# Optimization experiments

Measured on AMD Instinct MI355X. Metric: run time of the kernel, lower is better.

Reference implementation:

```python
import jax, jax.numpy as jnp
import numpy as np

B = 16      # number of point clouds
N = 4096    # points per cloud (max segment size, static)
D = 3       # xyz


def setup_inputs() -> dict:
    key = jax.random.key(0)
    k1, k2 = jax.random.split(key)
    pred = jax.random.normal(k1, (B * N, D), dtype=jnp.float32)
    target = jax.random.normal(k2, (B * N, D), dtype=jnp.float32)
    # sorted batch assignment with equal-size segments (so N_max is static)
    batch = jnp.repeat(jnp.arange(B, dtype=jnp.int64), N)
    return {"pred": pred, "target": target, "batch": batch}


def _to_dense_batch(x, batch):
    # Faithful to torch_geometric.utils.to_dense_batch: scatter each point into
    # its (cloud, within-cloud-position) slot; padding slots stay zero.
    T = x.shape[0]
    counts = jax.ops.segment_sum(jnp.ones((T,), jnp.int32), batch, num_segments=B)
    starts = jnp.concatenate([jnp.zeros((1,), jnp.int32), jnp.cumsum(counts)[:-1]])
    pos = jnp.arange(T, dtype=jnp.int32) - starts[batch]
    dense = jnp.zeros((B, N, x.shape[1]), x.dtype).at[batch, pos].set(x)
    return dense


def _chamfer(x, y):
    # pytorch3d.loss.chamfer_distance defaults: squared L2, point_reduction="mean",
    # batch_reduction="mean"; no lengths -> padded zeros count as points (as in source).
    x2 = jnp.sum(x * x, axis=-1)                      # [B, N]
    y2 = jnp.sum(y * y, axis=-1)                      # [B, N]
    xy = jnp.einsum("bid,bjd->bij", x, y)             # [B, N, N]
    d2 = x2[:, :, None] + y2[:, None, :] - 2.0 * xy   # [B, N, N] squared dists
    cham_x = jnp.mean(jnp.min(d2, axis=2), axis=1)    # x -> nearest y, mean over points
    cham_y = jnp.mean(jnp.min(d2, axis=1), axis=1)    # y -> nearest x
    return jnp.mean(cham_x + cham_y)                  # batch mean of summed directions


def reference(pred, target, batch):
    dense_x = _to_dense_batch(pred, batch)
    dense_y = _to_dense_batch(target, batch)
    return _chamfer(dense_x, dense_y)
```

## Files before the change

kernel.cpp:

```cpp
#include <hip/hip_runtime.h>


typedef __attribute__((ext_vector_type(8))) short bf16x8;
typedef __attribute__((ext_vector_type(16))) float floatx16;

#define BB 16
#define NN 4096
#define T  256
#define NPTS (BB * NN)
#define YC 512
#define NC (NN / YC)
#define XC 128
#define NXB (NN / XC)
#define NBLK (2 * BB * NXB)
#define ONEBF 0x3F80u

__device__ __forceinline__ unsigned int f2bf(float f) {
    unsigned int u = __float_as_uint(f);
    u += 0x7fffu + ((u >> 16) & 1u);
    return u >> 16;
}
__device__ __forceinline__ float bf2f(unsigned int h) {
    return __uint_as_float(h << 16);
}

__global__ __launch_bounds__(T) void chamfer_prep(
    const float* __restrict__ pred, const float* __restrict__ target,
    uint4* __restrict__ rec0, uint4* __restrict__ rec1)
{
    int g = blockIdx.x * T + threadIdx.x;
    int set = g >> 16;
    int idx = g & (NPTS - 1);
    const float* yp = (set ? pred : target) + (size_t)idx * 3;
    float y0 = yp[0], y1 = yp[1], y2 = yp[2];
    unsigned int h0 = f2bf(y0), h1 = f2bf(y1), h2 = f2bf(y2);
    unsigned int H0 = f2bf(-2.f * bf2f(h0));
    unsigned int H1 = f2bf(-2.f * bf2f(h1));
    unsigned int H2 = f2bf(-2.f * bf2f(h2));
    unsigned int L0 = f2bf(-2.f * (y0 - bf2f(h0)));
    unsigned int L1 = f2bf(-2.f * (y1 - bf2f(h1)));
    unsigned int L2 = f2bf(-2.f * (y2 - bf2f(h2)));
    float ysq = fmaf(y0, y0, fmaf(y1, y1, y2 * y2));
    unsigned int sh = f2bf(ysq);
    unsigned int sl = f2bf(ysq - bf2f(sh));
    rec0[g] = make_uint4(H0 | (H1 << 16), H2 | (H0 << 16),
                         H1 | (H2 << 16), L0 | (L1 << 16));
    rec1[g] = make_uint4(L2 | (ONEBF << 16), ONEBF | (sh << 16),
                         sl, 0u);
}

__global__ __launch_bounds__(T, 2) void chamfer_main(
    const float* __restrict__ pred, const float* __restrict__ target,
    const uint4* __restrict__ rec0, const uint4* __restrict__ rec1,
    float* __restrict__ bsum)
{
    __shared__ uint4 ldsy[2][YC];
    __shared__ float wsum[4];

    const int xb  = blockIdx.x;
    const int b   = blockIdx.y;
    const int dir = blockIdx.z;
    const float* xsrc = (dir ? target : pred) + (size_t)b * NN * 3;
    const size_t ygbase = (size_t)dir * NPTS + (size_t)b * NN;
    const int tid  = threadIdx.x;
    const int lane = tid & 63, w = tid >> 6;
    const int kg   = lane >> 5, m = lane & 31;

    union U { uint4 q; bf16x8 v; };
    U au;
    {
        int xi = xb * XC + w * 32 + m;
        const float* xp = xsrc + (size_t)xi * 3;
        float x0 = xp[0], x1 = xp[1], x2 = xp[2];
        unsigned int h0 = f2bf(x0), h1 = f2bf(x1), h2 = f2bf(x2);
        unsigned int L0 = f2bf(x0 - bf2f(h0));
        unsigned int L1 = f2bf(x1 - bf2f(h1));
        unsigned int L2 = f2bf(x2 - bf2f(h2));
        float xsq = fmaf(x0, x0, fmaf(x1, x1, x2 * x2));
        unsigned int sh = f2bf(xsq);
        unsigned int sl = f2bf(xsq - bf2f(sh));
        au.q = make_uint4(kg ? (h2 | (sh << 16))    : (h0 | (h1 << 16)),
                          kg ? (sl | (ONEBF << 16)) : (h2 | (L0 << 16)),
                          kg ? ONEBF                : (L1 | (L2 << 16)),
                          kg ? 0u                   : (h0 | (h1 << 16)));
    }

    floatx16 acc, zacc;
#pragma unroll
    for (int r = 0; r < 16; ++r) { acc[r] = 3.402823466e38f; zacc[r] = 0.f; }

    for (int c = 0; c < NC; ++c) {
        __syncthreads();
        for (int i = tid; i < YC; i += T) {
            ldsy[0][i] = rec0[ygbase + c * YC + i];
            ldsy[1][i] = rec1[ygbase + c * YC + i];
        }
        __syncthreads();
#pragma unroll 2
        for (int t = 0; t < YC / 32; t += 2) {
            U bu0, bu1;
            bu0.q = ldsy[kg][t * 32 + m];
            bu1.q = ldsy[kg][t * 32 + 32 + m];
            floatx16 d0 = __builtin_amdgcn_mfma_f32_32x32x16_bf16(
                au.v, bu0.v, zacc, 0, 0, 0);
            floatx16 d1 = __builtin_amdgcn_mfma_f32_32x32x16_bf16(
                au.v, bu1.v, zacc, 0, 0, 0);
#pragma unroll
            for (int r = 0; r < 16; ++r)
                acc[r] = fminf(fminf(acc[r], d0[r]), d1[r]);
        }
    }

    float s = 0.f;
#pragma unroll
    for (int r = 0; r < 16; ++r) {
        float v = acc[r];
        v = fminf(v, __shfl_xor(v, 1, 64));
        v = fminf(v, __shfl_xor(v, 2, 64));
        v = fminf(v, __shfl_xor(v, 4, 64));
        v = fminf(v, __shfl_xor(v, 8, 64));
        v = fminf(v, __shfl_xor(v, 16, 64));
        s += fmaxf(v, 0.f);
    }
    s += __shfl_xor(s, 32, 64);
    if (lane == 0) wsum[w] = s;
    __syncthreads();
    if (tid == 0)
        bsum[(dir * BB + b) * NXB + xb] = wsum[0] + wsum[1] + wsum[2] + wsum[3];
}

__global__ __launch_bounds__(T) void chamfer_final(
    const float* __restrict__ bsum, float* __restrict__ out)
{
    float s = 0.f;
    for (int i = threadIdx.x; i < NBLK; i += T) s += bsum[i];
#pragma unroll
    for (int off = 32; off > 0; off >>= 1)
        s += __shfl_down(s, off, 64);
    __shared__ float wsum[4];
    if ((threadIdx.x & 63) == 0) wsum[threadIdx.x >> 6] = s;
    __syncthreads();
    if (threadIdx.x == 0)
        out[0] = (wsum[0] + wsum[1] + wsum[2] + wsum[3]) * (1.0f / (BB * NN));
}

extern "C" void kernel_launch(void* const* d_in, const int* in_sizes, int n_in,
                              void* d_out, int out_size, void* d_ws, size_t ws_size,
                              hipStream_t stream) {
    const float* pred   = (const float*)d_in[0];
    const float* target = (const float*)d_in[1];
    float* out  = (float*)d_out;
    uint4* rec0 = (uint4*)d_ws;
    uint4* rec1 = rec0 + 2 * NPTS;
    float* bsum = (float*)(rec1 + 2 * NPTS);

    chamfer_prep<<<2 * NPTS / T, T, 0, stream>>>(pred, target, rec0, rec1);
    dim3 grid(NXB, BB, 2);
    chamfer_main<<<grid, T, 0, stream>>>(pred, target, rec0, rec1, bsum);
    chamfer_final<<<1, T, 0, stream>>>(bsum, out);
}
```

Before: 85.88 us.

## Double-buffer Y staging with direct global-to-LDS async loads

Replaces the synchronous register-staged copy of Y records into LDS with global_load_lds direct transfers into a double buffer, prefetching the next chunk while the MFMA loop runs on the current one. Manual vmcnt/lgkmcnt waits and raw barriers replace the __syncthreads pairs. Launch bounds occupancy hint is raised from 2 to 4 blocks per CU. This is meant to hide global load latency behind compute, at the cost of doubled LDS usage and fragile hand-written wait counts.

```diff
diff --git a/kernel.cpp b/kernel.cpp
--- a/kernel.cpp
+++ b/kernel.cpp
@@ -22,6 +22,12 @@
 }
 __device__ __forceinline__ float bf2f(unsigned int h) {
     return __uint_as_float(h << 16);
+}
+
+__device__ __forceinline__ void gl_lds16(const uint4* g, uint4* l) {
+    __builtin_amdgcn_global_load_lds(
+        (const __attribute__((address_space(1))) void*)g,
+        (__attribute__((address_space(3))) void*)l, 16, 0, 0);
 }
 
 __global__ __launch_bounds__(T) void chamfer_prep(
@@ -49,12 +55,21 @@
                          sl, 0u);
 }
 
-__global__ __launch_bounds__(T, 2) void chamfer_main(
+__device__ __forceinline__ void stage4(const uint4* __restrict__ r0,
+                                       const uint4* __restrict__ r1,
+                                       uint4* dst, int tid) {
+    gl_lds16(r0 + tid,       dst + tid);
+    gl_lds16(r0 + 256 + tid, dst + 256 + tid);
+    gl_lds16(r1 + tid,       dst + YC + tid);
+    gl_lds16(r1 + 256 + tid, dst + YC + 256 + tid);
+}
+
+__global__ __launch_bounds__(T, 4) void chamfer_main(
     const float* __restrict__ pred, const float* __restrict__ target,
     const uint4* __restrict__ rec0, const uint4* __restrict__ rec1,
     float* __restrict__ bsum)
 {
-    __shared__ uint4 ldsy[2][YC];
+    __shared__ uint4 ldsy[2][2][YC];
     __shared__ float wsum[4];
 
     const int xb  = blockIdx.x;
@@ -65,6 +80,11 @@
     const int tid  = threadIdx.x;
     const int lane = tid & 63, w = tid >> 6;
     const int kg   = lane >> 5, m = lane & 31;
+
+    const uint4* r0 = rec0 + ygbase;
+    const uint4* r1 = rec1 + ygbase;
+
+    stage4(r0, r1, &ldsy[0][0][0], tid);
 
     union U { uint4 q; bf16x8 v; };
     U au;
@@ -90,17 +110,21 @@
     for (int r = 0; r < 16; ++r) { acc[r] = 3.402823466e38f; zacc[r] = 0.f; }
 
     for (int c = 0; c < NC; ++c) {
-        __syncthreads();
-        for (int i = tid; i < YC; i += T) {
-            ldsy[0][i] = rec0[ygbase + c * YC + i];
-            ldsy[1][i] = rec1[ygbase + c * YC + i];
+        const int buf = c & 1;
+        if (c + 1 < NC) {
+            stage4(r0 + (c + 1) * YC, r1 + (c + 1) * YC,
+                   &ldsy[buf ^ 1][0][0], tid);
+            asm volatile("s_waitcnt vmcnt(4)" ::: "memory");
+        } else {
+            asm volatile("s_waitcnt vmcnt(0)" ::: "memory");
         }
-        __syncthreads();
+        __builtin_amdgcn_s_barrier();
+
 #pragma unroll 2
         for (int t = 0; t < YC / 32; t += 2) {
             U bu0, bu1;
-            bu0.q = ldsy[kg][t * 32 + m];
-            bu1.q = ldsy[kg][t * 32 + 32 + m];
+            bu0.q = ldsy[buf][kg][t * 32 + m];
+            bu1.q = ldsy[buf][kg][t * 32 + 32 + m];
             floatx16 d0 = __builtin_amdgcn_mfma_f32_32x32x16_bf16(
                 au.v, bu0.v, zacc, 0, 0, 0);
             floatx16 d1 = __builtin_amdgcn_mfma_f32_32x32x16_bf16(
@@ -109,6 +133,9 @@
             for (int r = 0; r < 16; ++r)
                 acc[r] = fminf(fminf(acc[r], d0[r]), d1[r]);
         }
+
+        asm volatile("s_waitcnt lgkmcnt(0)" ::: "memory");
+        __builtin_amdgcn_s_barrier();
     }
 
     float s = 0.f;
```

New measurement: 86.06 us. About the same (+0.2%).
